# Kernel tuning notes

Hardware: AMD Instinct MI355X
Metric: run time of the kernel (lower is better)

## Reference

```python
import jax, jax.numpy as jnp
import numpy as np

N_NODES = 10000
N_EDGES = 640000
IN_CH, HID, OUT_CH = 128, 128, 64


def _gcn_conv(x, edge_index, edge_weight, W, b, n_nodes):
    # PyG GCNConv (default add_self_loops=True, normalize=True, bias=True):
    #   A_hat = A + I ; D = rowsum(A_hat) ; norm_e = D^-1/2[src] * w_e * D^-1/2[dst]
    #   out[dst] += norm_e * (x @ W)[src] ; out += b
    src, dst = edge_index[0], edge_index[1]
    loop = jnp.arange(n_nodes, dtype=edge_index.dtype)
    src = jnp.concatenate([src, loop])
    dst = jnp.concatenate([dst, loop])
    w = jnp.concatenate([edge_weight, jnp.ones((n_nodes,), edge_weight.dtype)])
    deg = jax.ops.segment_sum(w, dst, num_segments=n_nodes)  # scatter on col
    dinv = jnp.where(deg > 0, jax.lax.rsqrt(deg), 0.0).astype(x.dtype)
    norm = dinv[src] * w * dinv[dst]  # [E+N]
    xw = x @ W  # dense GEMM [N, out]
    msg = norm[:, None] * xw[src]  # gather + scale [E+N, out]
    out = jax.ops.segment_sum(msg, dst, num_segments=n_nodes)  # scatter-add
    return out + b


def setup_inputs() -> dict:
    key = jax.random.key(0)
    ks = jax.random.split(key, 8)
    x = jax.random.normal(ks[0], (N_NODES, IN_CH), dtype=jnp.float32)
    edge_index = jax.random.randint(ks[1], (2, N_EDGES), 0, N_NODES, dtype=jnp.int64)
    edge_weight = jax.random.uniform(ks[2], (N_EDGES,), dtype=jnp.float32)
    W1 = jax.random.normal(ks[3], (IN_CH, HID), dtype=jnp.float32) * 0.05
    b1 = jnp.zeros((HID,), jnp.float32)
    W2 = jax.random.normal(ks[4], (HID, OUT_CH), dtype=jnp.float32) * 0.05
    b2 = jnp.zeros((OUT_CH,), jnp.float32)
    return {"x": x, "edge_index": edge_index, "edge_weight": edge_weight,
            "W1": W1, "b1": b1, "W2": W2, "b2": b2}


def reference(x, edge_index, edge_weight, W1, b1, W2, b2):
    h = _gcn_conv(x, edge_index, edge_weight, W1, b1, N_NODES)
    h = jax.nn.relu(h)
    out = _gcn_conv(h, edge_index, edge_weight, W2, b2, N_NODES)
    return out
```

## Files before the change

### kernel.cpp

```cpp
#include <hip/hip_runtime.h>
#include <math.h>

#define N_NODES 10000
#define N_EDGES 640000
#define ELLW    192

#define CHUNKS  128
#define CHUNK_E 5000
#define GB      625

typedef unsigned long long ull;
typedef unsigned int uint;
typedef unsigned short ushort;
typedef unsigned char uchar;

#define FIXED_SCALE 262144.0f


__device__ __forceinline__ float bf_lo(uint u) { return __uint_as_float(u << 16); }
__device__ __forceinline__ float bf_hi(uint u) { return __uint_as_float(u & 0xffff0000u); }
__device__ __forceinline__ ushort f2bf(float v) {
    uint u = __float_as_uint(v);
    uint r = u + 0x7fffu + ((u >> 16) & 1u);
    return (ushort)(r >> 16);
}

__global__ __launch_bounds__(256) void kernelA(const int* __restrict__ ei,
                                               const float* __restrict__ ew,
                                               uint* __restrict__ sd32,
                                               uint* __restrict__ blockcnt,
                                               const float* __restrict__ x,
                                               const float* __restrict__ W1,
                                               ushort* __restrict__ xw1b) {
    __shared__ __align__(16) uint smem[N_NODES];
    const int tid = threadIdx.x;
    if (blockIdx.x < CHUNKS) {
        const int c = blockIdx.x;
        __shared__ int sflag;
        if (tid == 0) sflag = 0;
        for (int i = tid; i < N_NODES; i += 256) smem[i] = 0u;
        __syncthreads();
        int a = (tid < 64) ? ei[2 * (c * CHUNK_E + tid) + 1] : 0;
        if (a) atomicOr(&sflag, 1);
        __syncthreads();
        const int f = sflag;
        const ull* ei64 = (const ull*)ei;
        for (int k = tid; k < CHUNK_E; k += 256) {
            int e = c * CHUNK_E + k;
            int s, d;
            if (f) { s = ei[e];        d = ei[N_EDGES + e]; }
            else   { s = (int)ei64[e]; d = (int)ei64[N_EDGES + e]; }
            float w = ew[e];
            uint fx = (uint)(w * FIXED_SCALE + 0.5f);
            uint old = atomicAdd(&smem[d], (1u << 24) | fx);
            uint r = (old >> 24) & 15u;
            sd32[e] = (r << 28) | ((uint)d << 14) | (uint)s;
        }
        __syncthreads();
        for (int i = tid; i < N_NODES; i += 256)
            blockcnt[c * N_NODES + i] = smem[i];
    } else {
        constexpr int K = 128, TM = 16, KT = 32, NCOL = 128, RPT = 8, LDA = KT + 4;
        float* sA = (float*)smem;
        float* sB = sA + TM * LDA;
        int blk = blockIdx.x - CHUNKS;
        int c = tid % NCOL, rr = tid / NCOL;
        int row0 = blk * TM;
        float acc[RPT];
#pragma unroll
        for (int r = 0; r < RPT; ++r) acc[r] = 0.0f;
        for (int k0 = 0; k0 < K; k0 += KT) {
            for (int i = tid; i < TM * KT; i += 256) {
                int r = i / KT, k = i % KT;
                int gr = row0 + r;
                sA[r * LDA + k] = (gr < N_NODES) ? x[gr * K + k0 + k] : 0.0f;
            }
            for (int i = tid; i < KT * NCOL; i += 256) {
                int k = i / NCOL, cc = i % NCOL;
                sB[k * NCOL + cc] = W1[(k0 + k) * NCOL + cc];
            }
            __syncthreads();
#pragma unroll
            for (int k = 0; k < KT; k += 4) {
                float b0 = sB[(k + 0) * NCOL + c];
                float b1 = sB[(k + 1) * NCOL + c];
                float b2 = sB[(k + 2) * NCOL + c];
                float b3 = sB[(k + 3) * NCOL + c];
#pragma unroll
                for (int r = 0; r < RPT; ++r) {
                    const float4 av = *(const float4*)&sA[(rr * RPT + r) * LDA + k];
                    acc[r] = fmaf(av.x, b0, acc[r]);
                    acc[r] = fmaf(av.y, b1, acc[r]);
                    acc[r] = fmaf(av.z, b2, acc[r]);
                    acc[r] = fmaf(av.w, b3, acc[r]);
                }
            }
            __syncthreads();
        }
#pragma unroll
        for (int r = 0; r < RPT; ++r) {
            int gr = row0 + rr * RPT + r;
            if (gr < N_NODES) xw1b[gr * NCOL + c] = f2bf(acc[r]);
        }
    }
}

__global__ __launch_bounds__(256) void scanB(const uint* __restrict__ blockcnt,
                                             uchar* __restrict__ base8,
                                             int* __restrict__ cnt_arr,
                                             float* __restrict__ dinv,
                                             const float* __restrict__ W2,
                                             uint* __restrict__ w2pg) {
    if (blockIdx.x >= 40) {
        int i = (blockIdx.x - 40) * 256 + threadIdx.x;
        int k2 = i >> 6, cc = i & 63;
        uint lo = (uint)f2bf(W2[(2 * k2) * 64 + cc]);
        uint hi = (uint)f2bf(W2[(2 * k2 + 1) * 64 + cc]);
        w2pg[i] = lo | (hi << 16);
        return;
    }
    int n = blockIdx.x * 256 + threadIdx.x;
    if (n >= N_NODES) return;
    uint wsum = 0;
    int run = 0;
#pragma unroll 8
    for (int c = 0; c < CHUNKS; ++c) {
        uint v = blockcnt[c * N_NODES + n];
        base8[c * N_NODES + n] = (uchar)run;
        run += (int)(v >> 24);
        wsum += v & 0xffffffu;
    }
    cnt_arr[n] = run;
    float dg = 1.0f + (float)wsum * (1.0f / FIXED_SCALE);
    dinv[n] = (float)(1.0 / sqrt((double)dg));
}

__global__ __launch_bounds__(256) void fillC(const uint* __restrict__ sd32,
                                             const float* __restrict__ ew,
                                             const uchar* __restrict__ base8,
                                             const float* __restrict__ dinv,
                                             ull* __restrict__ epack) {
    const int gid = blockIdx.x * 256 + threadIdx.x;
    const int stride = gridDim.x * 256;
    for (int e = gid; e < N_EDGES; e += stride) {
        uint sd = sd32[e];
        int s = (int)(sd & 0x3fffu);
        int d = (int)((sd >> 14) & 0x3fffu);
        int r = (int)(sd >> 28);
        int c = e / CHUNK_E;
        float nrm = dinv[s] * ew[e] * dinv[d];
        int slot = (int)base8[c * N_NODES + d] + r;
        if (slot < ELLW)
            epack[d * ELLW + slot] = ((ull)__float_as_uint(nrm) << 32) | (ull)(uint)s;
    }
}

__global__ __launch_bounds__(256, 4) void aggC(const ushort* __restrict__ xw1b,
                                               const ull* __restrict__ epack,
                                               const int* __restrict__ cnt_arr,
                                               const float* __restrict__ dinv,
                                               const float* __restrict__ b1,
                                               const uint* __restrict__ w2pg,
                                               ushort* __restrict__ xw2b) {
    __shared__ float hl[4][128];
    __shared__ uint w2p[64 * 64];
    const uint* __restrict__ xw32 = (const uint*)xw1b;
    const int tid = threadIdx.x;
    int l = tid & 63;
    int wv = tid >> 6;
    int node = blockIdx.x * 4 + wv;

    int cnt = __builtin_amdgcn_readfirstlane(cnt_arr[node]);
    if (cnt > ELLW) cnt = ELLW;
    const ull* ep = epack + (long)node * ELLW;

    ulonglong2 c0, c1, c2, c3;
    const bool has8 = (cnt >= 8);
    if (has8) {
        c0 = *(const ulonglong2*)(ep + 0);
        c1 = *(const ulonglong2*)(ep + 2);
        c2 = *(const ulonglong2*)(ep + 4);
        c3 = *(const ulonglong2*)(ep + 6);
    }

    for (int i = tid; i < 64 * 64; i += 256) w2p[i] = w2pg[i];

    float dn = dinv[node];
    float d2 = dn * dn;
    uint su = xw32[node * 64 + l];
    float acc0 = d2 * bf_lo(su);
    float acc1 = d2 * bf_hi(su);

    int j = 0;
    if (has8) {
        for (; j + 16 <= cnt; j += 8) {
            uint u0 = xw32[(uint)c0.x * 64 + l];
            uint u1 = xw32[(uint)c0.y * 64 + l];
            uint u2 = xw32[(uint)c1.x * 64 + l];
            uint u3 = xw32[(uint)c1.y * 64 + l];
            uint u4 = xw32[(uint)c2.x * 64 + l];
            uint u5 = xw32[(uint)c2.y * 64 + l];
            uint u6 = xw32[(uint)c3.x * 64 + l];
            uint u7 = xw32[(uint)c3.y * 64 + l];
            ulonglong2 p0 = *(const ulonglong2*)(ep + j + 8);
            ulonglong2 p1 = *(const ulonglong2*)(ep + j + 10);
            ulonglong2 p2 = *(const ulonglong2*)(ep + j + 12);
            ulonglong2 p3 = *(const ulonglong2*)(ep + j + 14);
            float n0 = __uint_as_float((uint)(c0.x >> 32));
            float n1 = __uint_as_float((uint)(c0.y >> 32));
            float n2 = __uint_as_float((uint)(c1.x >> 32));
            float n3 = __uint_as_float((uint)(c1.y >> 32));
            float n4 = __uint_as_float((uint)(c2.x >> 32));
            float n5 = __uint_as_float((uint)(c2.y >> 32));
            float n6 = __uint_as_float((uint)(c3.x >> 32));
            float n7 = __uint_as_float((uint)(c3.y >> 32));
            acc0 = fmaf(n0, bf_lo(u0), acc0); acc1 = fmaf(n0, bf_hi(u0), acc1);
            acc0 = fmaf(n1, bf_lo(u1), acc0); acc1 = fmaf(n1, bf_hi(u1), acc1);
            acc0 = fmaf(n2, bf_lo(u2), acc0); acc1 = fmaf(n2, bf_hi(u2), acc1);
            acc0 = fmaf(n3, bf_lo(u3), acc0); acc1 = fmaf(n3, bf_hi(u3), acc1);
            acc0 = fmaf(n4, bf_lo(u4), acc0); acc1 = fmaf(n4, bf_hi(u4), acc1);
            acc0 = fmaf(n5, bf_lo(u5), acc0); acc1 = fmaf(n5, bf_hi(u5), acc1);
            acc0 = fmaf(n6, bf_lo(u6), acc0); acc1 = fmaf(n6, bf_hi(u6), acc1);
            acc0 = fmaf(n7, bf_lo(u7), acc0); acc1 = fmaf(n7, bf_hi(u7), acc1);
            c0 = p0; c1 = p1; c2 = p2; c3 = p3;
        }
        {
            uint u0 = xw32[(uint)c0.x * 64 + l];
            uint u1 = xw32[(uint)c0.y * 64 + l];
            uint u2 = xw32[(uint)c1.x * 64 + l];
            uint u3 = xw32[(uint)c1.y * 64 + l];
            uint u4 = xw32[(uint)c2.x * 64 + l];
            uint u5 = xw32[(uint)c2.y * 64 + l];
            uint u6 = xw32[(uint)c3.x * 64 + l];
            uint u7 = xw32[(uint)c3.y * 64 + l];
            float n0 = __uint_as_float((uint)(c0.x >> 32));
            float n1 = __uint_as_float((uint)(c0.y >> 32));
            float n2 = __uint_as_float((uint)(c1.x >> 32));
            float n3 = __uint_as_float((uint)(c1.y >> 32));
            float n4 = __uint_as_float((uint)(c2.x >> 32));
            float n5 = __uint_as_float((uint)(c2.y >> 32));
            float n6 = __uint_as_float((uint)(c3.x >> 32));
            float n7 = __uint_as_float((uint)(c3.y >> 32));
            acc0 = fmaf(n0, bf_lo(u0), acc0); acc1 = fmaf(n0, bf_hi(u0), acc1);
            acc0 = fmaf(n1, bf_lo(u1), acc0); acc1 = fmaf(n1, bf_hi(u1), acc1);
            acc0 = fmaf(n2, bf_lo(u2), acc0); acc1 = fmaf(n2, bf_hi(u2), acc1);
            acc0 = fmaf(n3, bf_lo(u3), acc0); acc1 = fmaf(n3, bf_hi(u3), acc1);
            acc0 = fmaf(n4, bf_lo(u4), acc0); acc1 = fmaf(n4, bf_hi(u4), acc1);
            acc0 = fmaf(n5, bf_lo(u5), acc0); acc1 = fmaf(n5, bf_hi(u5), acc1);
            acc0 = fmaf(n6, bf_lo(u6), acc0); acc1 = fmaf(n6, bf_hi(u6), acc1);
            acc0 = fmaf(n7, bf_lo(u7), acc0); acc1 = fmaf(n7, bf_hi(u7), acc1);
            j += 8;
        }
    }
    for (; j + 2 <= cnt; j += 2) {
        ulonglong2 vv = *(const ulonglong2*)(ep + j);
        uint u0 = xw32[(uint)vv.x * 64 + l];
        uint u1 = xw32[(uint)vv.y * 64 + l];
        float n0 = __uint_as_float((uint)(vv.x >> 32));
        float n1 = __uint_as_float((uint)(vv.y >> 32));
        acc0 = fmaf(n0, bf_lo(u0), acc0); acc1 = fmaf(n0, bf_hi(u0), acc1);
        acc0 = fmaf(n1, bf_lo(u1), acc0); acc1 = fmaf(n1, bf_hi(u1), acc1);
    }
    if (j < cnt) {
        ull v = ep[j];
        uint u = xw32[(uint)v * 64 + l];
        float n = __uint_as_float((uint)(v >> 32));
        acc0 = fmaf(n, bf_lo(u), acc0);
        acc1 = fmaf(n, bf_hi(u), acc1);
    }
    float2 bb = ((const float2*)b1)[l];
    hl[wv][2 * l]     = fmaxf(acc0 + bb.x, 0.0f);
    hl[wv][2 * l + 1] = fmaxf(acc1 + bb.y, 0.0f);
    __syncthreads();

    float acc = 0.0f;
#pragma unroll 8
    for (int k2 = 0; k2 < 64; ++k2) {
        uint w = w2p[k2 * 64 + l];
        acc = fmaf(hl[wv][2 * k2],     bf_lo(w), acc);
        acc = fmaf(hl[wv][2 * k2 + 1], bf_hi(w), acc);
    }
    xw2b[node * 64 + l] = f2bf(acc);
}

__global__ __launch_bounds__(256) void agg2(const ushort* __restrict__ xw2b,
                                            const ull* __restrict__ epack,
                                            const int* __restrict__ cnt_arr,
                                            const float* __restrict__ dinv,
                                            const float* __restrict__ b2,
                                            float* __restrict__ out) {
    const uint* __restrict__ xw32 = (const uint*)xw2b;
    int lane = threadIdx.x & 63;
    int half = lane >> 5;
    int q = lane & 31;
    int pair = blockIdx.x * 4 + (threadIdx.x >> 6);
    int A = pair * 2, B = A + 1;
    int cntA = __builtin_amdgcn_readfirstlane(cnt_arr[A]);
    int cntB = __builtin_amdgcn_readfirstlane(cnt_arr[B]);
    if (cntA > ELLW) cntA = ELLW;
    if (cntB > ELLW) cntB = ELLW;
    int myn = half ? B : A;
    int mycnt = half ? cntB : cntA;
    float dn = dinv[myn];
    float d2 = dn * dn;
    uint su = xw32[myn * 32 + q];
    float acc0 = d2 * bf_lo(su);
    float acc1 = d2 * bf_hi(su);
    const ull* ep = epack + (long)myn * ELLW;
    int mx = cntA > cntB ? cntA : cntB;
    int j = 0;
    if (mx >= 8) {
        ulonglong2 c0 = *(const ulonglong2*)(ep + 0);
        ulonglong2 c1 = *(const ulonglong2*)(ep + 2);
        ulonglong2 c2 = *(const ulonglong2*)(ep + 4);
        ulonglong2 c3 = *(const ulonglong2*)(ep + 6);
        for (; j + 16 <= mx; j += 8) {
            uint u0 = xw32[((uint)c0.x & 0xffffu) * 32 + q];
            uint u1 = xw32[((uint)c0.y & 0xffffu) * 32 + q];
            uint u2 = xw32[((uint)c1.x & 0xffffu) * 32 + q];
            uint u3 = xw32[((uint)c1.y & 0xffffu) * 32 + q];
            uint u4 = xw32[((uint)c2.x & 0xffffu) * 32 + q];
            uint u5 = xw32[((uint)c2.y & 0xffffu) * 32 + q];
            uint u6 = xw32[((uint)c3.x & 0xffffu) * 32 + q];
            uint u7 = xw32[((uint)c3.y & 0xffffu) * 32 + q];
            ulonglong2 p0 = *(const ulonglong2*)(ep + j + 8);
            ulonglong2 p1 = *(const ulonglong2*)(ep + j + 10);
            ulonglong2 p2 = *(const ulonglong2*)(ep + j + 12);
            ulonglong2 p3 = *(const ulonglong2*)(ep + j + 14);
            float n0 = (j     < mycnt) ? __uint_as_float((uint)(c0.x >> 32)) : 0.0f;
            float n1 = (j + 1 < mycnt) ? __uint_as_float((uint)(c0.y >> 32)) : 0.0f;
            float n2 = (j + 2 < mycnt) ? __uint_as_float((uint)(c1.x >> 32)) : 0.0f;
            float n3 = (j + 3 < mycnt) ? __uint_as_float((uint)(c1.y >> 32)) : 0.0f;
            float n4 = (j + 4 < mycnt) ? __uint_as_float((uint)(c2.x >> 32)) : 0.0f;
            float n5 = (j + 5 < mycnt) ? __uint_as_float((uint)(c2.y >> 32)) : 0.0f;
            float n6 = (j + 6 < mycnt) ? __uint_as_float((uint)(c3.x >> 32)) : 0.0f;
            float n7 = (j + 7 < mycnt) ? __uint_as_float((uint)(c3.y >> 32)) : 0.0f;
            acc0 = fmaf(n0, bf_lo(u0), acc0); acc1 = fmaf(n0, bf_hi(u0), acc1);
            acc0 = fmaf(n1, bf_lo(u1), acc0); acc1 = fmaf(n1, bf_hi(u1), acc1);
            acc0 = fmaf(n2, bf_lo(u2), acc0); acc1 = fmaf(n2, bf_hi(u2), acc1);
            acc0 = fmaf(n3, bf_lo(u3), acc0); acc1 = fmaf(n3, bf_hi(u3), acc1);
            acc0 = fmaf(n4, bf_lo(u4), acc0); acc1 = fmaf(n4, bf_hi(u4), acc1);
            acc0 = fmaf(n5, bf_lo(u5), acc0); acc1 = fmaf(n5, bf_hi(u5), acc1);
            acc0 = fmaf(n6, bf_lo(u6), acc0); acc1 = fmaf(n6, bf_hi(u6), acc1);
            acc0 = fmaf(n7, bf_lo(u7), acc0); acc1 = fmaf(n7, bf_hi(u7), acc1);
            c0 = p0; c1 = p1; c2 = p2; c3 = p3;
        }
        {
            uint u0 = xw32[((uint)c0.x & 0xffffu) * 32 + q];
            uint u1 = xw32[((uint)c0.y & 0xffffu) * 32 + q];
            uint u2 = xw32[((uint)c1.x & 0xffffu) * 32 + q];
            uint u3 = xw32[((uint)c1.y & 0xffffu) * 32 + q];
            uint u4 = xw32[((uint)c2.x & 0xffffu) * 32 + q];
            uint u5 = xw32[((uint)c2.y & 0xffffu) * 32 + q];
            uint u6 = xw32[((uint)c3.x & 0xffffu) * 32 + q];
            uint u7 = xw32[((uint)c3.y & 0xffffu) * 32 + q];
            float n0 = (j     < mycnt) ? __uint_as_float((uint)(c0.x >> 32)) : 0.0f;
            float n1 = (j + 1 < mycnt) ? __uint_as_float((uint)(c0.y >> 32)) : 0.0f;
            float n2 = (j + 2 < mycnt) ? __uint_as_float((uint)(c1.x >> 32)) : 0.0f;
            float n3 = (j + 3 < mycnt) ? __uint_as_float((uint)(c1.y >> 32)) : 0.0f;
            float n4 = (j + 4 < mycnt) ? __uint_as_float((uint)(c2.x >> 32)) : 0.0f;
            float n5 = (j + 5 < mycnt) ? __uint_as_float((uint)(c2.y >> 32)) : 0.0f;
            float n6 = (j + 6 < mycnt) ? __uint_as_float((uint)(c3.x >> 32)) : 0.0f;
            float n7 = (j + 7 < mycnt) ? __uint_as_float((uint)(c3.y >> 32)) : 0.0f;
            acc0 = fmaf(n0, bf_lo(u0), acc0); acc1 = fmaf(n0, bf_hi(u0), acc1);
            acc0 = fmaf(n1, bf_lo(u1), acc0); acc1 = fmaf(n1, bf_hi(u1), acc1);
            acc0 = fmaf(n2, bf_lo(u2), acc0); acc1 = fmaf(n2, bf_hi(u2), acc1);
            acc0 = fmaf(n3, bf_lo(u3), acc0); acc1 = fmaf(n3, bf_hi(u3), acc1);
            acc0 = fmaf(n4, bf_lo(u4), acc0); acc1 = fmaf(n4, bf_hi(u4), acc1);
            acc0 = fmaf(n5, bf_lo(u5), acc0); acc1 = fmaf(n5, bf_hi(u5), acc1);
            acc0 = fmaf(n6, bf_lo(u6), acc0); acc1 = fmaf(n6, bf_hi(u6), acc1);
            acc0 = fmaf(n7, bf_lo(u7), acc0); acc1 = fmaf(n7, bf_hi(u7), acc1);
            j += 8;
        }
    }
    for (; j < mx; ++j) {
        ull v = ep[j];
        uint s = (uint)v & 0xffffu;
        float n = (j < mycnt) ? __uint_as_float((uint)(v >> 32)) : 0.0f;
        uint u = xw32[s * 32 + q];
        acc0 = fmaf(n, bf_lo(u), acc0);
        acc1 = fmaf(n, bf_hi(u), acc1);
    }
    float2 bb = ((const float2*)b2)[q];
    float2 o;
    o.x = acc0 + bb.x;
    o.y = acc1 + bb.y;
    ((float2*)out)[myn * 32 + q] = o;
}

extern "C" void kernel_launch(void* const* d_in, const int* in_sizes, int n_in,
                              void* d_out, int out_size, void* d_ws, size_t ws_size,
                              hipStream_t stream) {
    const float* x  = (const float*)d_in[0];
    const int*   ei = (const int*)d_in[1];
    const float* ew = (const float*)d_in[2];
    const float* W1 = (const float*)d_in[3];
    const float* b1 = (const float*)d_in[4];
    const float* W2 = (const float*)d_in[5];
    const float* b2 = (const float*)d_in[6];
    float* out = (float*)d_out;

    char* ws = (char*)d_ws;
    ushort* xw1b    = (ushort*)(ws + 0);
    ushort* xw2b    = (ushort*)(ws + 5120000);
    ull*    epack   = (ull*)   (ws + 6400000);
    uint*   blockcnt= (uint*)  (ws + 21760000);
    uchar*  base8   = (uchar*) (ws + 26880000);
    uint*   sd32    = (uint*)  (ws + 28800000);
    int*    cnt_arr = (int*)   (ws + 31360000);
    float*  dinv    = (float*) (ws + 31400000);
    uint*   w2pg    = (uint*)  (ws + 31440000);

    kernelA<<<CHUNKS + GB, 256, 0, stream>>>(ei, ew, sd32, blockcnt, x, W1, xw1b);
    scanB<<<56, 256, 0, stream>>>(blockcnt, base8, cnt_arr, dinv, W2, w2pg);
    fillC<<<2500, 256, 0, stream>>>(sd32, ew, base8, dinv, epack);
    aggC<<<2500, 256, 0, stream>>>(xw1b, epack, cnt_arr, dinv, b1, w2pg, xw2b);
    agg2<<<1250, 256, 0, stream>>>(xw2b, epack, cnt_arr, dinv, b2, out);
}
```

Baseline: 146.7 us.

## Build ELL adjacency with global 64-bit atomics and apply degree normalization in aggregation

Drops the per-chunk shared-memory histogram, the prefix scan over 128 chunks and the separate fill pass. Each edge now does one 64-bit global atomicAdd that packs the slot count and the fixed-point weight sum, then writes its ELL entry straight away with the raw weight. The symmetric normalization is factored out: the aggregation kernels multiply by dinv[src] per edge and by dinv[dst] once at the end. This removes two kernels and the large blockcnt/base8 traffic, at the cost of contended global atomics, a nondeterministic slot order, and an extra gathered dinv load per edge.

New measurement: 182.2 us. 24.2% more time.

```diff
diff --git a/kernel.cpp b/kernel.cpp
--- a/kernel.cpp
+++ b/kernel.cpp
@@ -5,8 +5,7 @@
 #define N_EDGES 640000
 #define ELLW    192
 
-#define CHUNKS  128
-#define CHUNK_E 5000
+#define FB      2500
 #define GB      625
 
 typedef unsigned long long ull;
@@ -15,6 +14,7 @@
 typedef unsigned char uchar;
 
 #define FIXED_SCALE 262144.0f
+#define WMASK 0xFFFFFFFFFFFULL
 
 
 __device__ __forceinline__ float bf_lo(uint u) { return __uint_as_float(u << 16); }
@@ -25,45 +25,55 @@
     return (ushort)(r >> 16);
 }
 
-__global__ __launch_bounds__(256) void kernelA(const int* __restrict__ ei,
-                                               const float* __restrict__ ew,
-                                               uint* __restrict__ sd32,
-                                               uint* __restrict__ blockcnt,
-                                               const float* __restrict__ x,
-                                               const float* __restrict__ W1,
-                                               ushort* __restrict__ xw1b) {
-    __shared__ __align__(16) uint smem[N_NODES];
+__global__ __launch_bounds__(256) void prepK(ull* __restrict__ deg64,
+                                             const float* __restrict__ W2,
+                                             uint* __restrict__ w2pg) {
+    if (blockIdx.x < 40) {
+        int n = blockIdx.x * 256 + threadIdx.x;
+        if (n < N_NODES) deg64[n] = 0ULL;
+    } else {
+        int i = (blockIdx.x - 40) * 256 + threadIdx.x;
+        int k2 = i >> 6, cc = i & 63;
+        uint lo = (uint)f2bf(W2[(2 * k2) * 64 + cc]);
+        uint hi = (uint)f2bf(W2[(2 * k2 + 1) * 64 + cc]);
+        w2pg[i] = lo | (hi << 16);
+    }
+}
+
+__global__ __launch_bounds__(256) void fillgemm(const int* __restrict__ ei,
+                                                const float* __restrict__ ew,
+                                                ull* __restrict__ deg64,
+                                                ull* __restrict__ epack,
+                                                const float* __restrict__ x,
+                                                const float* __restrict__ W1,
+                                                ushort* __restrict__ xw1b) {
+    __shared__ __align__(16) float smem[16 * 36 + 32 * 128];
+    __shared__ int sflag;
     const int tid = threadIdx.x;
-    if (blockIdx.x < CHUNKS) {
-        const int c = blockIdx.x;
-        __shared__ int sflag;
+    if (blockIdx.x < FB) {
+        const int e0 = blockIdx.x * 256;
         if (tid == 0) sflag = 0;
-        for (int i = tid; i < N_NODES; i += 256) smem[i] = 0u;
         __syncthreads();
-        int a = (tid < 64) ? ei[2 * (c * CHUNK_E + tid) + 1] : 0;
+        int a = (tid < 64) ? ei[2 * (e0 + tid) + 1] : 0;
         if (a) atomicOr(&sflag, 1);
         __syncthreads();
         const int f = sflag;
         const ull* ei64 = (const ull*)ei;
-        for (int k = tid; k < CHUNK_E; k += 256) {
-            int e = c * CHUNK_E + k;
-            int s, d;
-            if (f) { s = ei[e];        d = ei[N_EDGES + e]; }
-            else   { s = (int)ei64[e]; d = (int)ei64[N_EDGES + e]; }
-            float w = ew[e];
-            uint fx = (uint)(w * FIXED_SCALE + 0.5f);
-            uint old = atomicAdd(&smem[d], (1u << 24) | fx);
-            uint r = (old >> 24) & 15u;
-            sd32[e] = (r << 28) | ((uint)d << 14) | (uint)s;
-        }
-        __syncthreads();
-        for (int i = tid; i < N_NODES; i += 256)
-            blockcnt[c * N_NODES + i] = smem[i];
+        int e = e0 + tid;
+        int s, d;
+        if (f) { s = ei[e];        d = ei[N_EDGES + e]; }
+        else   { s = (int)ei64[e]; d = (int)ei64[N_EDGES + e]; }
+        float w = ew[e];
+        uint wfix = (uint)(w * FIXED_SCALE + 0.5f);
+        ull old = atomicAdd(&deg64[d], (1ULL << 44) | (ull)wfix);
+        uint slot = (uint)(old >> 44);
+        if (slot < ELLW)
+            epack[(long)d * ELLW + slot] = ((ull)__float_as_uint(w) << 32) | (ull)(uint)s;
     } else {
         constexpr int K = 128, TM = 16, KT = 32, NCOL = 128, RPT = 8, LDA = KT + 4;
-        float* sA = (float*)smem;
-        float* sB = sA + TM * LDA;
-        int blk = blockIdx.x - CHUNKS;
+        float* sA = smem;
+        float* sB = smem + TM * LDA;
+        int blk = blockIdx.x - FB;
         int c = tid % NCOL, rr = tid / NCOL;
         int row0 = blk * TM;
         float acc[RPT];
@@ -105,54 +115,15 @@
     }
 }
 
-__global__ __launch_bounds__(256) void scanB(const uint* __restrict__ blockcnt,
-                                             uchar* __restrict__ base8,
+__global__ __launch_bounds__(256) void dinvK(const ull* __restrict__ deg64,
                                              int* __restrict__ cnt_arr,
-                                             float* __restrict__ dinv,
-                                             const float* __restrict__ W2,
-                                             uint* __restrict__ w2pg) {
-    if (blockIdx.x >= 40) {
-        int i = (blockIdx.x - 40) * 256 + threadIdx.x;
-        int k2 = i >> 6, cc = i & 63;
-        uint lo = (uint)f2bf(W2[(2 * k2) * 64 + cc]);
-        uint hi = (uint)f2bf(W2[(2 * k2 + 1) * 64 + cc]);
-        w2pg[i] = lo | (hi << 16);
-        return;
-    }
+                                             float* __restrict__ dinv) {
     int n = blockIdx.x * 256 + threadIdx.x;
     if (n >= N_NODES) return;
-    uint wsum = 0;
-    int run = 0;
-#pragma unroll 8
-    for (int c = 0; c < CHUNKS; ++c) {
-        uint v = blockcnt[c * N_NODES + n];
-        base8[c * N_NODES + n] = (uchar)run;
-        run += (int)(v >> 24);
-        wsum += v & 0xffffffu;
-    }
-    cnt_arr[n] = run;
-    float dg = 1.0f + (float)wsum * (1.0f / FIXED_SCALE);
+    ull v = deg64[n];
+    cnt_arr[n] = (int)(v >> 44);
+    float dg = 1.0f + (float)(v & WMASK) * (1.0f / FIXED_SCALE);
     dinv[n] = (float)(1.0 / sqrt((double)dg));
-}
-
-__global__ __launch_bounds__(256) void fillC(const uint* __restrict__ sd32,
-                                             const float* __restrict__ ew,
-                                             const uchar* __restrict__ base8,
-                                             const float* __restrict__ dinv,
-                                             ull* __restrict__ epack) {
-    const int gid = blockIdx.x * 256 + threadIdx.x;
-    const int stride = gridDim.x * 256;
-    for (int e = gid; e < N_EDGES; e += stride) {
-        uint sd = sd32[e];
-        int s = (int)(sd & 0x3fffu);
-        int d = (int)((sd >> 14) & 0x3fffu);
-        int r = (int)(sd >> 28);
-        int c = e / CHUNK_E;
-        float nrm = dinv[s] * ew[e] * dinv[d];
-        int slot = (int)base8[c * N_NODES + d] + r;
-        if (slot < ELLW)
-            epack[d * ELLW + slot] = ((ull)__float_as_uint(nrm) << 32) | (ull)(uint)s;
-    }
 }
 
 __global__ __launch_bounds__(256, 4) void aggC(const ushort* __restrict__ xw1b,
@@ -186,14 +157,21 @@
     for (int i = tid; i < 64 * 64; i += 256) w2p[i] = w2pg[i];
 
     float dn = dinv[node];
-    float d2 = dn * dn;
     uint su = xw32[node * 64 + l];
-    float acc0 = d2 * bf_lo(su);
-    float acc1 = d2 * bf_hi(su);
+    float acc0 = dn * bf_lo(su);
+    float acc1 = dn * bf_hi(su);
 
     int j = 0;
     if (has8) {
         for (; j + 16 <= cnt; j += 8) {
+            float m0 = __uint_as_float((uint)(c0.x >> 32)) * dinv[(uint)c0.x];
+            float m1 = __uint_as_float((uint)(c0.y >> 32)) * dinv[(uint)c0.y];
+            float m2 = __uint_as_float((uint)(c1.x >> 32)) * dinv[(uint)c1.x];
+            float m3 = __uint_as_float((uint)(c1.y >> 32)) * dinv[(uint)c1.y];
+            float m4 = __uint_as_float((uint)(c2.x >> 32)) * dinv[(uint)c2.x];
+            float m5 = __uint_as_float((uint)(c2.y >> 32)) * dinv[(uint)c2.y];
+            float m6 = __uint_as_float((uint)(c3.x >> 32)) * dinv[(uint)c3.x];
+            float m7 = __uint_as_float((uint)(c3.y >> 32)) * dinv[(uint)c3.y];
             uint u0 = xw32[(uint)c0.x * 64 + l];
             uint u1 = xw32[(uint)c0.y * 64 + l];
             uint u2 = xw32[(uint)c1.x * 64 + l];
@@ -206,25 +184,25 @@
             ulonglong2 p1 = *(const ulonglong2*)(ep + j + 10);
             ulonglong2 p2 = *(const ulonglong2*)(ep + j + 12);
             ulonglong2 p3 = *(const ulonglong2*)(ep + j + 14);
-            float n0 = __uint_as_float((uint)(c0.x >> 32));
-            float n1 = __uint_as_float((uint)(c0.y >> 32));
-            float n2 = __uint_as_float((uint)(c1.x >> 32));
-            float n3 = __uint_as_float((uint)(c1.y >> 32));
-            float n4 = __uint_as_float((uint)(c2.x >> 32));
-            float n5 = __uint_as_float((uint)(c2.y >> 32));
-            float n6 = __uint_as_float((uint)(c3.x >> 32));
-            float n7 = __uint_as_float((uint)(c3.y >> 32));
-            acc0 = fmaf(n0, bf_lo(u0), acc0); acc1 = fmaf(n0, bf_hi(u0), acc1);
-            acc0 = fmaf(n1, bf_lo(u1), acc0); acc1 = fmaf(n1, bf_hi(u1), acc1);
-            acc0 = fmaf(n2, bf_lo(u2), acc0); acc1 = fmaf(n2, bf_hi(u2), acc1);
-            acc0 = fmaf(n3, bf_lo(u3), acc0); acc1 = fmaf(n3, bf_hi(u3), acc1);
-            acc0 = fmaf(n4, bf_lo(u4), acc0); acc1 = fmaf(n4, bf_hi(u4), acc1);
-            acc0 = fmaf(n5, bf_lo(u5), acc0); acc1 = fmaf(n5, bf_hi(u5), acc1);
-            acc0 = fmaf(n6, bf_lo(u6), acc0); acc1 = fmaf(n6, bf_hi(u6), acc1);
-            acc0 = fmaf(n7, bf_lo(u7), acc0); acc1 = fmaf(n7, bf_hi(u7), acc1);
+            acc0 = fmaf(m0, bf_lo(u0), acc0); acc1 = fmaf(m0, bf_hi(u0), acc1);
+            acc0 = fmaf(m1, bf_lo(u1), acc0); acc1 = fmaf(m1, bf_hi(u1), acc1);
+            acc0 = fmaf(m2, bf_lo(u2), acc0); acc1 = fmaf(m2, bf_hi(u2), acc1);
+            acc0 = fmaf(m3, bf_lo(u3), acc0); acc1 = fmaf(m3, bf_hi(u3), acc1);
+            acc0 = fmaf(m4, bf_lo(u4), acc0); acc1 = fmaf(m4, bf_hi(u4), acc1);
+            acc0 = fmaf(m5, bf_lo(u5), acc0); acc1 = fmaf(m5, bf_hi(u5), acc1);
+            acc0 = fmaf(m6, bf_lo(u6), acc0); acc1 = fmaf(m6, bf_hi(u6), acc1);
+            acc0 = fmaf(m7, bf_lo(u7), acc0); acc1 = fmaf(m7, bf_hi(u7), acc1);
             c0 = p0; c1 = p1; c2 = p2; c3 = p3;
         }
         {
+            float m0 = __uint_as_float((uint)(c0.x >> 32)) * dinv[(uint)c0.x];
+            float m1 = __uint_as_float((uint)(c0.y >> 32)) * dinv[(uint)c0.y];
+            float m2 = __uint_as_float((uint)(c1.x >> 32)) * dinv[(uint)c1.x];
+            float m3 = __uint_as_float((uint)(c1.y >> 32)) * dinv[(uint)c1.y];
+            float m4 = __uint_as_float((uint)(c2.x >> 32)) * dinv[(uint)c2.x];
+            float m5 = __uint_as_float((uint)(c2.y >> 32)) * dinv[(uint)c2.y];
+            float m6 = __uint_as_float((uint)(c3.x >> 32)) * dinv[(uint)c3.x];
+            float m7 = __uint_as_float((uint)(c3.y >> 32)) * dinv[(uint)c3.y];
             uint u0 = xw32[(uint)c0.x * 64 + l];
             uint u1 = xw32[(uint)c0.y * 64 + l];
             uint u2 = xw32[(uint)c1.x * 64 + l];
@@ -233,44 +211,36 @@
             uint u5 = xw32[(uint)c2.y * 64 + l];
             uint u6 = xw32[(uint)c3.x * 64 + l];
             uint u7 = xw32[(uint)c3.y * 64 + l];
-            float n0 = __uint_as_float((uint)(c0.x >> 32));
-            float n1 = __uint_as_float((uint)(c0.y >> 32));
-            float n2 = __uint_as_float((uint)(c1.x >> 32));
-            float n3 = __uint_as_float((uint)(c1.y >> 32));
-            float n4 = __uint_as_float((uint)(c2.x >> 32));
-            float n5 = __uint_as_float((uint)(c2.y >> 32));
-            float n6 = __uint_as_float((uint)(c3.x >> 32));
-            float n7 = __uint_as_float((uint)(c3.y >> 32));
-            acc0 = fmaf(n0, bf_lo(u0), acc0); acc1 = fmaf(n0, bf_hi(u0), acc1);
-            acc0 = fmaf(n1, bf_lo(u1), acc0); acc1 = fmaf(n1, bf_hi(u1), acc1);
-            acc0 = fmaf(n2, bf_lo(u2), acc0); acc1 = fmaf(n2, bf_hi(u2), acc1);
-            acc0 = fmaf(n3, bf_lo(u3), acc0); acc1 = fmaf(n3, bf_hi(u3), acc1);
-            acc0 = fmaf(n4, bf_lo(u4), acc0); acc1 = fmaf(n4, bf_hi(u4), acc1);
-            acc0 = fmaf(n5, bf_lo(u5), acc0); acc1 = fmaf(n5, bf_hi(u5), acc1);
-            acc0 = fmaf(n6, bf_lo(u6), acc0); acc1 = fmaf(n6, bf_hi(u6), acc1);
-            acc0 = fmaf(n7, bf_lo(u7), acc0); acc1 = fmaf(n7, bf_hi(u7), acc1);
+            acc0 = fmaf(m0, bf_lo(u0), acc0); acc1 = fmaf(m0, bf_hi(u0), acc1);
+            acc0 = fmaf(m1, bf_lo(u1), acc0); acc1 = fmaf(m1, bf_hi(u1), acc1);
+            acc0 = fmaf(m2, bf_lo(u2), acc0); acc1 = fmaf(m2, bf_hi(u2), acc1);
+            acc0 = fmaf(m3, bf_lo(u3), acc0); acc1 = fmaf(m3, bf_hi(u3), acc1);
+            acc0 = fmaf(m4, bf_lo(u4), acc0); acc1 = fmaf(m4, bf_hi(u4), acc1);
+            acc0 = fmaf(m5, bf_lo(u5), acc0); acc1 = fmaf(m5, bf_hi(u5), acc1);
+            acc0 = fmaf(m6, bf_lo(u6), acc0); acc1 = fmaf(m6, bf_hi(u6), acc1);
+            acc0 = fmaf(m7, bf_lo(u7), acc0); acc1 = fmaf(m7, bf_hi(u7), acc1);
             j += 8;
         }
     }
     for (; j + 2 <= cnt; j += 2) {
         ulonglong2 vv = *(const ulonglong2*)(ep + j);
+        float m0 = __uint_as_float((uint)(vv.x >> 32)) * dinv[(uint)vv.x];
+        float m1 = __uint_as_float((uint)(vv.y >> 32)) * dinv[(uint)vv.y];
         uint u0 = xw32[(uint)vv.x * 64 + l];
         uint u1 = xw32[(uint)vv.y * 64 + l];
-        float n0 = __uint_as_float((uint)(vv.x >> 32));
-        float n1 = __uint_as_float((uint)(vv.y >> 32));
-        acc0 = fmaf(n0, bf_lo(u0), acc0); acc1 = fmaf(n0, bf_hi(u0), acc1);
-        acc0 = fmaf(n1, bf_lo(u1), acc0); acc1 = fmaf(n1, bf_hi(u1), acc1);
+        acc0 = fmaf(m0, bf_lo(u0), acc0); acc1 = fmaf(m0, bf_hi(u0), acc1);
+        acc0 = fmaf(m1, bf_lo(u1), acc0); acc1 = fmaf(m1, bf_hi(u1), acc1);
     }
     if (j < cnt) {
         ull v = ep[j];
+        float m = __uint_as_float((uint)(v >> 32)) * dinv[(uint)v];
         uint u = xw32[(uint)v * 64 + l];
-        float n = __uint_as_float((uint)(v >> 32));
-        acc0 = fmaf(n, bf_lo(u), acc0);
-        acc1 = fmaf(n, bf_hi(u), acc1);
+        acc0 = fmaf(m, bf_lo(u), acc0);
+        acc1 = fmaf(m, bf_hi(u), acc1);
     }
     float2 bb = ((const float2*)b1)[l];
-    hl[wv][2 * l]     = fmaxf(acc0 + bb.x, 0.0f);
-    hl[wv][2 * l + 1] = fmaxf(acc1 + bb.y, 0.0f);
+    hl[wv][2 * l]     = fmaxf(fmaf(dn, acc0, bb.x), 0.0f);
+    hl[wv][2 * l + 1] = fmaxf(fmaf(dn, acc1, bb.y), 0.0f);
     __syncthreads();
 
     float acc = 0.0f;
@@ -302,10 +272,9 @@
     int myn = half ? B : A;
     int mycnt = half ? cntB : cntA;
     float dn = dinv[myn];
-    float d2 = dn * dn;
     uint su = xw32[myn * 32 + q];
-    float acc0 = d2 * bf_lo(su);
-    float acc1 = d2 * bf_hi(su);
+    float acc0 = dn * bf_lo(su);
+    float acc1 = dn * bf_hi(su);
     const ull* ep = epack + (long)myn * ELLW;
     int mx = cntA > cntB ? cntA : cntB;
     int j = 0;
@@ -315,76 +284,76 @@
         ulonglong2 c2 = *(const ulonglong2*)(ep + 4);
         ulonglong2 c3 = *(const ulonglong2*)(ep + 6);
         for (; j + 16 <= mx; j += 8) {
-            uint u0 = xw32[((uint)c0.x & 0xffffu) * 32 + q];
-            uint u1 = xw32[((uint)c0.y & 0xffffu) * 32 + q];
-            uint u2 = xw32[((uint)c1.x & 0xffffu) * 32 + q];
-            uint u3 = xw32[((uint)c1.y & 0xffffu) * 32 + q];
-            uint u4 = xw32[((uint)c2.x & 0xffffu) * 32 + q];
-            uint u5 = xw32[((uint)c2.y & 0xffffu) * 32 + q];
-            uint u6 = xw32[((uint)c3.x & 0xffffu) * 32 + q];
-            uint u7 = xw32[((uint)c3.y & 0xffffu) * 32 + q];
+            float m0 = (j     < mycnt) ? __uint_as_float((uint)(c0.x >> 32)) * dinv[(uint)c0.x & 0x3fffu] : 0.0f;
+            float m1 = (j + 1 < mycnt) ? __uint_as_float((uint)(c0.y >> 32)) * dinv[(uint)c0.y & 0x3fffu] : 0.0f;
+            float m2 = (j + 2 < mycnt) ? __uint_as_float((uint)(c1.x >> 32)) * dinv[(uint)c1.x & 0x3fffu] : 0.0f;
+            float m3 = (j + 3 < mycnt) ? __uint_as_float((uint)(c1.y >> 32)) * dinv[(uint)c1.y & 0x3fffu] : 0.0f;
+            float m4 = (j + 4 < mycnt) ? __uint_as_float((uint)(c2.x >> 32)) * dinv[(uint)c2.x & 0x3fffu] : 0.0f;
+            float m5 = (j + 5 < mycnt) ? __uint_as_float((uint)(c2.y >> 32)) * dinv[(uint)c2.y & 0x3fffu] : 0.0f;
+            float m6 = (j + 6 < mycnt) ? __uint_as_float((uint)(c3.x >> 32)) * dinv[(uint)c3.x & 0x3fffu] : 0.0f;
+            float m7 = (j + 7 < mycnt) ? __uint_as_float((uint)(c3.y >> 32)) * dinv[(uint)c3.y & 0x3fffu] : 0.0f;
+            uint u0 = xw32[((uint)c0.x & 0x3fffu) * 32 + q];
+            uint u1 = xw32[((uint)c0.y & 0x3fffu) * 32 + q];
+            uint u2 = xw32[((uint)c1.x & 0x3fffu) * 32 + q];
+            uint u3 = xw32[((uint)c1.y & 0x3fffu) * 32 + q];
+            uint u4 = xw32[((uint)c2.x & 0x3fffu) * 32 + q];
+            uint u5 = xw32[((uint)c2.y & 0x3fffu) * 32 + q];
+            uint u6 = xw32[((uint)c3.x & 0x3fffu) * 32 + q];
+            uint u7 = xw32[((uint)c3.y & 0x3fffu) * 32 + q];
             ulonglong2 p0 = *(const ulonglong2*)(ep + j + 8);
             ulonglong2 p1 = *(const ulonglong2*)(ep + j + 10);
             ulonglong2 p2 = *(const ulonglong2*)(ep + j + 12);
             ulonglong2 p3 = *(const ulonglong2*)(ep + j + 14);
-            float n0 = (j     < mycnt) ? __uint_as_float((uint)(c0.x >> 32)) : 0.0f;
-            float n1 = (j + 1 < mycnt) ? __uint_as_float((uint)(c0.y >> 32)) : 0.0f;
-            float n2 = (j + 2 < mycnt) ? __uint_as_float((uint)(c1.x >> 32)) : 0.0f;
-            float n3 = (j + 3 < mycnt) ? __uint_as_float((uint)(c1.y >> 32)) : 0.0f;
-            float n4 = (j + 4 < mycnt) ? __uint_as_float((uint)(c2.x >> 32)) : 0.0f;
-            float n5 = (j + 5 < mycnt) ? __uint_as_float((uint)(c2.y >> 32)) : 0.0f;
-            float n6 = (j + 6 < mycnt) ? __uint_as_float((uint)(c3.x >> 32)) : 0.0f;
-            float n7 = (j + 7 < mycnt) ? __uint_as_float((uint)(c3.y >> 32)) : 0.0f;
-            acc0 = fmaf(n0, bf_lo(u0), acc0); acc1 = fmaf(n0, bf_hi(u0), acc1);
-            acc0 = fmaf(n1, bf_lo(u1), acc0); acc1 = fmaf(n1, bf_hi(u1), acc1);
-            acc0 = fmaf(n2, bf_lo(u2), acc0); acc1 = fmaf(n2, bf_hi(u2), acc1);
-            acc0 = fmaf(n3, bf_lo(u3), acc0); acc1 = fmaf(n3, bf_hi(u3), acc1);
-            acc0 = fmaf(n4, bf_lo(u4), acc0); acc1 = fmaf(n4, bf_hi(u4), acc1);
-            acc0 = fmaf(n5, bf_lo(u5), acc0); acc1 = fmaf(n5, bf_hi(u5), acc1);
-            acc0 = fmaf(n6, bf_lo(u6), acc0); acc1 = fmaf(n6, bf_hi(u6), acc1);
-            acc0 = fmaf(n7, bf_lo(u7), acc0); acc1 = fmaf(n7, bf_hi(u7), acc1);
+            acc0 = fmaf(m0, bf_lo(u0), acc0); acc1 = fmaf(m0, bf_hi(u0), acc1);
+            acc0 = fmaf(m1, bf_lo(u1), acc0); acc1 = fmaf(m1, bf_hi(u1), acc1);
+            acc0 = fmaf(m2, bf_lo(u2), acc0); acc1 = fmaf(m2, bf_hi(u2), acc1);
+            acc0 = fmaf(m3, bf_lo(u3), acc0); acc1 = fmaf(m3, bf_hi(u3), acc1);
+            acc0 = fmaf(m4, bf_lo(u4), acc0); acc1 = fmaf(m4, bf_hi(u4), acc1);
+            acc0 = fmaf(m5, bf_lo(u5), acc0); acc1 = fmaf(m5, bf_hi(u5), acc1);
+            acc0 = fmaf(m6, bf_lo(u6), acc0); acc1 = fmaf(m6, bf_hi(u6), acc1);
+            acc0 = fmaf(m7, bf_lo(u7), acc0); acc1 = fmaf(m7, bf_hi(u7), acc1);
             c0 = p0; c1 = p1; c2 = p2; c3 = p3;
         }
         {
-            uint u0 = xw32[((uint)c0.x & 0xffffu) * 32 + q];
-            uint u1 = xw32[((uint)c0.y & 0xffffu) * 32 + q];
-            uint u2 = xw32[((uint)c1.x & 0xffffu) * 32 + q];
-            uint u3 = xw32[((uint)c1.y & 0xffffu) * 32 + q];
-            uint u4 = xw32[((uint)c2.x & 0xffffu) * 32 + q];
-            uint u5 = xw32[((uint)c2.y & 0xffffu) * 32 + q];
-            uint u6 = xw32[((uint)c3.x & 0xffffu) * 32 + q];
-            uint u7 = xw32[((uint)c3.y & 0xffffu) * 32 + q];
-            float n0 = (j     < mycnt) ? __uint_as_float((uint)(c0.x >> 32)) : 0.0f;
-            float n1 = (j + 1 < mycnt) ? __uint_as_float((uint)(c0.y >> 32)) : 0.0f;
-            float n2 = (j + 2 < mycnt) ? __uint_as_float((uint)(c1.x >> 32)) : 0.0f;
-            float n3 = (j + 3 < mycnt) ? __uint_as_float((uint)(c1.y >> 32)) : 0.0f;
-            float n4 = (j + 4 < mycnt) ? __uint_as_float((uint)(c2.x >> 32)) : 0.0f;
-            float n5 = (j + 5 < mycnt) ? __uint_as_float((uint)(c2.y >> 32)) : 0.0f;
-            float n6 = (j + 6 < mycnt) ? __uint_as_float((uint)(c3.x >> 32)) : 0.0f;
-            float n7 = (j + 7 < mycnt) ? __uint_as_float((uint)(c3.y >> 32)) : 0.0f;
-            acc0 = fmaf(n0, bf_lo(u0), acc0); acc1 = fmaf(n0, bf_hi(u0), acc1);
-            acc0 = fmaf(n1, bf_lo(u1), acc0); acc1 = fmaf(n1, bf_hi(u1), acc1);
-            acc0 = fmaf(n2, bf_lo(u2), acc0); acc1 = fmaf(n2, bf_hi(u2), acc1);
-            acc0 = fmaf(n3, bf_lo(u3), acc0); acc1 = fmaf(n3, bf_hi(u3), acc1);
-            acc0 = fmaf(n4, bf_lo(u4), acc0); acc1 = fmaf(n4, bf_hi(u4), acc1);
-            acc0 = fmaf(n5, bf_lo(u5), acc0); acc1 = fmaf(n5, bf_hi(u5), acc1);
-            acc0 = fmaf(n6, bf_lo(u6), acc0); acc1 = fmaf(n6, bf_hi(u6), acc1);
-            acc0 = fmaf(n7, bf_lo(u7), acc0); acc1 = fmaf(n7, bf_hi(u7), acc1);
+            float m0 = (j     < mycnt) ? __uint_as_float((uint)(c0.x >> 32)) * dinv[(uint)c0.x & 0x3fffu] : 0.0f;
+            float m1 = (j + 1 < mycnt) ? __uint_as_float((uint)(c0.y >> 32)) * dinv[(uint)c0.y & 0x3fffu] : 0.0f;
+            float m2 = (j + 2 < mycnt) ? __uint_as_float((uint)(c1.x >> 32)) * dinv[(uint)c1.x & 0x3fffu] : 0.0f;
+            float m3 = (j + 3 < mycnt) ? __uint_as_float((uint)(c1.y >> 32)) * dinv[(uint)c1.y & 0x3fffu] : 0.0f;
+            float m4 = (j + 4 < mycnt) ? __uint_as_float((uint)(c2.x >> 32)) * dinv[(uint)c2.x & 0x3fffu] : 0.0f;
+            float m5 = (j + 5 < mycnt) ? __uint_as_float((uint)(c2.y >> 32)) * dinv[(uint)c2.y & 0x3fffu] : 0.0f;
+            float m6 = (j + 6 < mycnt) ? __uint_as_float((uint)(c3.x >> 32)) * dinv[(uint)c3.x & 0x3fffu] : 0.0f;
+            float m7 = (j + 7 < mycnt) ? __uint_as_float((uint)(c3.y >> 32)) * dinv[(uint)c3.y & 0x3fffu] : 0.0f;
+            uint u0 = xw32[((uint)c0.x & 0x3fffu) * 32 + q];
+            uint u1 = xw32[((uint)c0.y & 0x3fffu) * 32 + q];
+            uint u2 = xw32[((uint)c1.x & 0x3fffu) * 32 + q];
+            uint u3 = xw32[((uint)c1.y & 0x3fffu) * 32 + q];
+            uint u4 = xw32[((uint)c2.x & 0x3fffu) * 32 + q];
+            uint u5 = xw32[((uint)c2.y & 0x3fffu) * 32 + q];
+            uint u6 = xw32[((uint)c3.x & 0x3fffu) * 32 + q];
+            uint u7 = xw32[((uint)c3.y & 0x3fffu) * 32 + q];
+            acc0 = fmaf(m0, bf_lo(u0), acc0); acc1 = fmaf(m0, bf_hi(u0), acc1);
+            acc0 = fmaf(m1, bf_lo(u1), acc0); acc1 = fmaf(m1, bf_hi(u1), acc1);
+            acc0 = fmaf(m2, bf_lo(u2), acc0); acc1 = fmaf(m2, bf_hi(u2), acc1);
+            acc0 = fmaf(m3, bf_lo(u3), acc0); acc1 = fmaf(m3, bf_hi(u3), acc1);
+            acc0 = fmaf(m4, bf_lo(u4), acc0); acc1 = fmaf(m4, bf_hi(u4), acc1);
+            acc0 = fmaf(m5, bf_lo(u5), acc0); acc1 = fmaf(m5, bf_hi(u5), acc1);
+            acc0 = fmaf(m6, bf_lo(u6), acc0); acc1 = fmaf(m6, bf_hi(u6), acc1);
+            acc0 = fmaf(m7, bf_lo(u7), acc0); acc1 = fmaf(m7, bf_hi(u7), acc1);
             j += 8;
         }
     }
     for (; j < mx; ++j) {
         ull v = ep[j];
-        uint s = (uint)v & 0xffffu;
-        float n = (j < mycnt) ? __uint_as_float((uint)(v >> 32)) : 0.0f;
+        uint s = (uint)v & 0x3fffu;
+        float m = (j < mycnt) ? __uint_as_float((uint)(v >> 32)) * dinv[s] : 0.0f;
         uint u = xw32[s * 32 + q];
-        acc0 = fmaf(n, bf_lo(u), acc0);
-        acc1 = fmaf(n, bf_hi(u), acc1);
+        acc0 = fmaf(m, bf_lo(u), acc0);
+        acc1 = fmaf(m, bf_hi(u), acc1);
     }
     float2 bb = ((const float2*)b2)[q];
     float2 o;
-    o.x = acc0 + bb.x;
-    o.y = acc1 + bb.y;
+    o.x = fmaf(dn, acc0, bb.x);
+    o.y = fmaf(dn, acc1, bb.y);
     ((float2*)out)[myn * 32 + q] = o;
 }
 
@@ -404,16 +373,14 @@
     ushort* xw1b    = (ushort*)(ws + 0);
     ushort* xw2b    = (ushort*)(ws + 5120000);
     ull*    epack   = (ull*)   (ws + 6400000);
-    uint*   blockcnt= (uint*)  (ws + 21760000);
-    uchar*  base8   = (uchar*) (ws + 26880000);
-    uint*   sd32    = (uint*)  (ws + 28800000);
-    int*    cnt_arr = (int*)   (ws + 31360000);
-    float*  dinv    = (float*) (ws + 31400000);
-    uint*   w2pg    = (uint*)  (ws + 31440000);
-
-    kernelA<<<CHUNKS + GB, 256, 0, stream>>>(ei, ew, sd32, blockcnt, x, W1, xw1b);
-    scanB<<<56, 256, 0, stream>>>(blockcnt, base8, cnt_arr, dinv, W2, w2pg);
-    fillC<<<2500, 256, 0, stream>>>(sd32, ew, base8, dinv, epack);
+    ull*    deg64   = (ull*)   (ws + 21760000);
+    int*    cnt_arr = (int*)   (ws + 21840000);
+    float*  dinv    = (float*) (ws + 21880000);
+    uint*   w2pg    = (uint*)  (ws + 21920000);
+
+    prepK<<<56, 256, 0, stream>>>(deg64, W2, w2pg);
+    fillgemm<<<FB + GB, 256, 0, stream>>>(ei, ew, deg64, epack, x, W1, xw1b);
+    dinvK<<<40, 256, 0, stream>>>(deg64, cnt_arr, dinv);
     aggC<<<2500, 256, 0, stream>>>(xw1b, epack, cnt_arr, dinv, b1, w2pg, xw2b);
     agg2<<<1250, 256, 0, stream>>>(xw2b, epack, cnt_arr, dinv, b2, out);
 }
```
